# Kernel tuning notes

Hardware: AMD Instinct MI355X
Metric: run time of the kernel (lower is better)

## Reference

```python
import jax, jax.numpy as jnp
import numpy as np

N, C, H = 256, 128, 4
D = C // H


def setup_inputs() -> dict:
    key = jax.random.key(0)
    ks = jax.random.split(key, 7)
    pair_rep = jax.random.normal(ks[0], (N, N, C), dtype=jnp.float32)
    distance_matrix = jax.random.normal(ks[1], (N, N), dtype=jnp.float32)
    Wqkv = jax.random.normal(ks[2], (C, 3 * C), dtype=jnp.float32) * (1.0 / np.sqrt(C))
    bqkv = jax.random.normal(ks[3], (3 * C,), dtype=jnp.float32) * 0.02
    Wout = jax.random.normal(ks[4], (C, C), dtype=jnp.float32) * (1.0 / np.sqrt(C))
    bout = jax.random.normal(ks[5], (C,), dtype=jnp.float32) * 0.02
    dscale = jnp.ones((1,), dtype=jnp.float32)
    mask = jax.random.randint(ks[6], (N, N), 0, 2).astype(jnp.bool_)
    return {"pair_rep": pair_rep, "distance_matrix": distance_matrix, "Wqkv": Wqkv,
            "bqkv": bqkv, "Wout": Wout, "bout": bout, "dscale": dscale, "mask": mask}


def reference(pair_rep, distance_matrix, Wqkv, bqkv, Wout, bout, dscale, mask):
    n = pair_rep.shape[0]
    qkv = pair_rep @ Wqkv + bqkv                      # [n,n,3c]
    q, k, v = jnp.split(qkv, 3, axis=-1)
    q = q.reshape(n, n, H, D)
    k = k.reshape(n, n, H, D)
    v = v.reshape(n, n, H, D)
    # scores[h,i,j,k] = q[i,j,h,:] . k[i,k,h,:] / sqrt(D)
    scores = jnp.einsum('ijhd,ikhd->hijk', q, k) / np.sqrt(D)
    bias = (dscale[0] * distance_matrix)[None, None, :, :]   # [1,1,n,n]
    scores = scores + bias
    scores = jnp.where(mask[None, None, :, :], -jnp.inf, scores)
    attn = jax.nn.softmax(scores, axis=-1)            # [H,n,n,n]
    out = jnp.einsum('hijk,ikhd->ijhd', attn, v).reshape(n, n, C)
    return out @ Wout + bout
```

## Files before the change

kernel.cpp:

```cpp
#include <hip/hip_runtime.h>
#include <hip/hip_bf16.h>
#include <math.h>

#define NN 256
#define CC 128
#define HH 4
#define DD 32

typedef uint4 u128;
typedef __bf16 bf16x8 __attribute__((ext_vector_type(8)));
typedef float f32x4 __attribute__((ext_vector_type(4)));

#define LOG2E 1.4426950408889634f
#define QSC (0.17677669529663687f * LOG2E)

__global__ __launch_bounds__(256) void prep_kernel(
    const float* __restrict__ dm, const int* __restrict__ mask,
    const float* __restrict__ dscale,
    const float* __restrict__ Wqkv, const float* __restrict__ Wout,
    float* __restrict__ biasM,
    __hip_bfloat16* __restrict__ Wt_qkv, __hip_bfloat16* __restrict__ Wt_out)
{
    const int b = blockIdx.x, t = threadIdx.x;
    if (b < 256) {
        int idx = b * 256 + t;
        biasM[idx] = mask[idx] ? -INFINITY : dscale[0] * dm[idx] * LOG2E;
    } else if (b < 448) {
        int idx = (b - 256) * 256 + t;
        int n = idx >> 7, k = idx & 127;
        Wt_qkv[idx] = __float2bfloat16(Wqkv[(size_t)k * 384 + n]);
    } else {
        int idx = (b - 448) * 256 + t;
        int n = idx >> 7, k = idx & 127;
        Wt_out[idx] = __float2bfloat16(Wout[(size_t)k * CC + n]);
    }
}

__global__ __launch_bounds__(512, 4) void qkv_mfma_kernel(
    const float* __restrict__ A,
    const __hip_bfloat16* __restrict__ Bt,
    const float* __restrict__ bias,
    __hip_bfloat16* __restrict__ out)
{
    __shared__ __align__(16) __hip_bfloat16 As[128][136];
    __shared__ __align__(16) __hip_bfloat16 Bs[96][136];
    const int t = threadIdx.x;
    const int m0 = blockIdx.x * 128;
    const int n0 = blockIdx.y * 96;

    #pragma unroll
    for (int it = 0; it < 8; ++it) {
        int idx = it * 512 + t;
        int r = idx >> 5, c4 = (idx & 31) * 4;
        float4 v = *(const float4*)(A + (size_t)(m0 + r) * CC + c4);
        __hip_bfloat162 a01 = __float22bfloat162_rn(float2{v.x, v.y});
        __hip_bfloat162 a23 = __float22bfloat162_rn(float2{v.z, v.w});
        uint2 pk;
        pk.x = *(unsigned int*)&a01;
        pk.y = *(unsigned int*)&a23;
        *(uint2*)&As[r][c4] = pk;
    }
    #pragma unroll
    for (int it = 0; it < 3; ++it) {
        int idx = it * 512 + t;
        int n = idx >> 4, c8 = (idx & 15) * 8;
        *(u128*)&Bs[n][c8] = *(const u128*)(Bt + (size_t)(n0 + n) * CC + c8);
    }
    __syncthreads();

    const int w = t >> 6, lane = t & 63;
    const int n16 = lane & 15, quad = lane >> 4;
    const int mw = (w & 3) * 32, nw = (w >> 2) * 48;

    bf16x8 pf[2][4];
    #pragma unroll
    for (int mt = 0; mt < 2; ++mt)
        #pragma unroll
        for (int ks = 0; ks < 4; ++ks)
            pf[mt][ks] = *(const bf16x8*)&As[mw + mt * 16 + n16][ks * 32 + quad * 8];

    f32x4 acc[2][3];
    #pragma unroll
    for (int mt = 0; mt < 2; ++mt)
        #pragma unroll
        for (int nt = 0; nt < 3; ++nt) acc[mt][nt] = (f32x4){0.f, 0.f, 0.f, 0.f};

    #pragma unroll
    for (int nt = 0; nt < 3; ++nt) {
        bf16x8 wf[4];
        #pragma unroll
        for (int ks = 0; ks < 4; ++ks)
            wf[ks] = *(const bf16x8*)&Bs[nw + nt * 16 + n16][ks * 32 + quad * 8];
        #pragma unroll
        for (int ks = 0; ks < 4; ++ks)
            #pragma unroll
            for (int mt = 0; mt < 2; ++mt)
                acc[mt][nt] = __builtin_amdgcn_mfma_f32_16x16x32_bf16(wf[ks], pf[mt][ks], acc[mt][nt], 0, 0, 0);
    }

    #pragma unroll
    for (int nt = 0; nt < 3; ++nt) {
        int nbase = n0 + nw + nt * 16 + quad * 4;
        float4 b4 = *(const float4*)(bias + nbase);
        float sc = (nbase < CC) ? QSC : 1.0f;
        #pragma unroll
        for (int mt = 0; mt < 2; ++mt) {
            int m = m0 + mw + mt * 16 + n16;
            __hip_bfloat162 h01 = __float22bfloat162_rn(float2{(acc[mt][nt][0] + b4.x) * sc, (acc[mt][nt][1] + b4.y) * sc});
            __hip_bfloat162 h23 = __float22bfloat162_rn(float2{(acc[mt][nt][2] + b4.z) * sc, (acc[mt][nt][3] + b4.w) * sc});
            uint2 pk;
            pk.x = *(unsigned int*)&h01;
            pk.y = *(unsigned int*)&h23;
            *(uint2*)&out[(size_t)m * 384 + nbase] = pk;
        }
    }
}

__global__ __launch_bounds__(512, 4) void attn_mfma_kernel(
    const __hip_bfloat16* __restrict__ qkv,
    const float* __restrict__ biasM,
    __hip_bfloat16* __restrict__ attn_out)
{
    __shared__ __align__(16) __hip_bfloat16 Ks[NN][40];
    __shared__ __align__(16) __hip_bfloat16 VTs[DD][264];
    __shared__ __align__(16) __hip_bfloat16 Ps[8][16][136];

    const int bi = blockIdx.x;
    const int i = bi >> 2, h = bi & 3;
    const int t = threadIdx.x;

    if (t < NN) {
        const __hip_bfloat16* base = qkv + (size_t)(i * NN + t) * 384 + h * DD;
        const u128* ksrc = (const u128*)(base + CC);
        const u128* vsrc = (const u128*)(base + 2 * CC);
        u128* kdst = (u128*)&Ks[t][0];
        u128 vr[4];
        #pragma unroll
        for (int u = 0; u < 4; ++u) { kdst[u] = ksrc[u]; vr[u] = vsrc[u]; }
        const __hip_bfloat16* vh = (const __hip_bfloat16*)vr;
        #pragma unroll
        for (int d = 0; d < DD; ++d) VTs[d][t] = vh[d];
    }
    __syncthreads();

    const int w = t >> 6, lane = t & 63;
    const int n16 = lane & 15, quad = lane >> 4;

    for (int jt = 0; jt < 2; ++jt) {
        const int j0 = w * 32 + jt * 16;
        const int j = j0 + n16;

        bf16x8 qa = *(const bf16x8*)(qkv + (size_t)(i * NN + j) * 384 + h * DD + quad * 8);
        const float4* brow = (const float4*)(biasM + (size_t)j * NN);

        f32x4 s[16];
        #pragma unroll
        for (int kt = 0; kt < 16; ++kt) {
            bf16x8 kb = *(const bf16x8*)&Ks[kt * 16 + n16][quad * 8];
            float4 b4 = brow[kt * 4 + quad];
            s[kt] = __builtin_amdgcn_mfma_f32_16x16x32_bf16(
                kb, qa, (f32x4){b4.x, b4.y, b4.z, b4.w}, 0, 0, 0);
        }

        f32x4 sm = {0.f, 0.f, 0.f, 0.f};
        f32x4 o[2] = {(f32x4){0.f, 0.f, 0.f, 0.f}, (f32x4){0.f, 0.f, 0.f, 0.f}};
        #pragma unroll
        for (int pass = 0; pass < 2; ++pass) {
            #pragma unroll
            for (int kt8 = 0; kt8 < 8; ++kt8) {
                int kt = pass * 8 + kt8;
                float p0 = exp2f(s[kt][0]);
                float p1 = exp2f(s[kt][1]);
                float p2 = exp2f(s[kt][2]);
                float p3 = exp2f(s[kt][3]);
                sm[0] += p0; sm[1] += p1; sm[2] += p2; sm[3] += p3;
                __hip_bfloat162 h01 = __float22bfloat162_rn(float2{p0, p1});
                __hip_bfloat162 h23 = __float22bfloat162_rn(float2{p2, p3});
                uint2 pk;
                pk.x = *(unsigned int*)&h01;
                pk.y = *(unsigned int*)&h23;
                *(uint2*)&Ps[w][n16][kt8 * 16 + quad * 4] = pk;
            }
            #pragma unroll
            for (int c = 0; c < 4; ++c) {
                bf16x8 pa = *(const bf16x8*)&Ps[w][n16][c * 32 + quad * 8];
                #pragma unroll
                for (int dt = 0; dt < 2; ++dt) {
                    bf16x8 vb = *(const bf16x8*)&VTs[dt * 16 + n16][pass * 128 + c * 32 + quad * 8];
                    o[dt] = __builtin_amdgcn_mfma_f32_16x16x32_bf16(vb, pa, o[dt], 0, 0, 0);
                }
            }
        }
        float sum = (sm[0] + sm[1]) + (sm[2] + sm[3]);
        sum += __shfl_xor(sum, 16);
        sum += __shfl_xor(sum, 32);
        float inv = 1.0f / sum;

        __hip_bfloat16* obase = attn_out + (size_t)(i * NN + j) * CC + h * DD + quad * 4;
        #pragma unroll
        for (int dt = 0; dt < 2; ++dt) {
            __hip_bfloat162 h01 = __float22bfloat162_rn(float2{o[dt][0] * inv, o[dt][1] * inv});
            __hip_bfloat162 h23 = __float22bfloat162_rn(float2{o[dt][2] * inv, o[dt][3] * inv});
            uint2 pk;
            pk.x = *(unsigned int*)&h01;
            pk.y = *(unsigned int*)&h23;
            *(uint2*)(obase + dt * 16) = pk;
        }
    }
}

__global__ __launch_bounds__(512, 4) void out_mfma_kernel(
    const __hip_bfloat16* __restrict__ A,
    const __hip_bfloat16* __restrict__ Bt,
    const float* __restrict__ bias,
    float* __restrict__ out)
{
    __shared__ __align__(16) __hip_bfloat16 As[128][136];
    __shared__ __align__(16) __hip_bfloat16 Bs[128][136];
    const int t = threadIdx.x;
    const int m0 = blockIdx.x * 128;

    #pragma unroll
    for (int it = 0; it < 4; ++it) {
        int idx = it * 512 + t;
        int r = idx >> 4, c8 = (idx & 15) * 8;
        *(u128*)&As[r][c8] = *(const u128*)(A + (size_t)(m0 + r) * CC + c8);
    }
    #pragma unroll
    for (int it = 0; it < 4; ++it) {
        int idx = it * 512 + t;
        int n = idx >> 4, c8 = (idx & 15) * 8;
        *(u128*)&Bs[n][c8] = *(const u128*)(Bt + (size_t)n * CC + c8);
    }
    __syncthreads();

    const int w = t >> 6, lane = t & 63;
    const int n16 = lane & 15, quad = lane >> 4;
    const int mw = (w & 3) * 32, nw = (w >> 2) * 64;

    bf16x8 pf[2][4];
    #pragma unroll
    for (int mt = 0; mt < 2; ++mt)
        #pragma unroll
        for (int ks = 0; ks < 4; ++ks)
            pf[mt][ks] = *(const bf16x8*)&As[mw + mt * 16 + n16][ks * 32 + quad * 8];

    f32x4 acc[2][4];
    #pragma unroll
    for (int mt = 0; mt < 2; ++mt)
        #pragma unroll
        for (int nt = 0; nt < 4; ++nt) acc[mt][nt] = (f32x4){0.f, 0.f, 0.f, 0.f};

    #pragma unroll
    for (int nt = 0; nt < 4; ++nt) {
        bf16x8 wf[4];
        #pragma unroll
        for (int ks = 0; ks < 4; ++ks)
            wf[ks] = *(const bf16x8*)&Bs[nw + nt * 16 + n16][ks * 32 + quad * 8];
        #pragma unroll
        for (int ks = 0; ks < 4; ++ks)
            #pragma unroll
            for (int mt = 0; mt < 2; ++mt)
                acc[mt][nt] = __builtin_amdgcn_mfma_f32_16x16x32_bf16(wf[ks], pf[mt][ks], acc[mt][nt], 0, 0, 0);
    }

    #pragma unroll
    for (int nt = 0; nt < 4; ++nt) {
        int nbase = nw + nt * 16 + quad * 4;
        float4 b4 = *(const float4*)(bias + nbase);
        #pragma unroll
        for (int mt = 0; mt < 2; ++mt) {
            int m = m0 + mw + mt * 16 + n16;
            float4 ov;
            ov.x = acc[mt][nt][0] + b4.x;
            ov.y = acc[mt][nt][1] + b4.y;
            ov.z = acc[mt][nt][2] + b4.z;
            ov.w = acc[mt][nt][3] + b4.w;
            *(float4*)&out[(size_t)m * CC + nbase] = ov;
        }
    }
}

extern "C" void kernel_launch(void* const* d_in, const int* in_sizes, int n_in,
                              void* d_out, int out_size, void* d_ws, size_t ws_size,
                              hipStream_t stream) {
    const float* pair_rep = (const float*)d_in[0];
    const float* dm       = (const float*)d_in[1];
    const float* Wqkv     = (const float*)d_in[2];
    const float* bqkv     = (const float*)d_in[3];
    const float* Wout     = (const float*)d_in[4];
    const float* bout     = (const float*)d_in[5];
    const float* dscale   = (const float*)d_in[6];
    const int*   mask     = (const int*)d_in[7];
    float* out = (float*)d_out;

    char* p = (char*)d_ws;
    float* biasM = (float*)p;                 p += (size_t)NN * NN * 4;
    __hip_bfloat16* Wt_qkv = (__hip_bfloat16*)p;  p += (size_t)384 * CC * 2;
    __hip_bfloat16* Wt_out = (__hip_bfloat16*)p;  p += (size_t)CC * CC * 2;
    __hip_bfloat16* qkv  = (__hip_bfloat16*)p;    p += (size_t)65536 * 384 * 2;
    __hip_bfloat16* attn = (__hip_bfloat16*)p;

    prep_kernel<<<dim3(512), dim3(256), 0, stream>>>(dm, mask, dscale, Wqkv, Wout, biasM, Wt_qkv, Wt_out);
    qkv_mfma_kernel<<<dim3(512, 4), dim3(512), 0, stream>>>(pair_rep, Wt_qkv, bqkv, qkv);
    attn_mfma_kernel<<<dim3(1024), dim3(512), 0, stream>>>(qkv, biasM, attn);
    out_mfma_kernel<<<dim3(512), dim3(512), 0, stream>>>(attn, Wt_out, bout, out);
}
```

Measured before the change: 173.3 us.

## Shrink GEMM tiles, read weights from global directly, parallelize K/V staging

The QKV and output projection kernels now use 64-row tiles with 256 threads and twice as many blocks. Weight fragments are loaded straight from global memory (L2/L1-cached) instead of being staged in shared memory, which cuts LDS usage and removes a staging pass. The attention kernel now loads K/V with all 512 threads, two per row, instead of half the block, and unrolls the jt loop. The trade-off is more repeated global weight reads across blocks and less reuse of each weight fragment across row tiles.

```diff
diff --git a/kernel.cpp b/kernel.cpp
--- a/kernel.cpp
+++ b/kernel.cpp
@@ -36,21 +36,20 @@
     }
 }
 
-__global__ __launch_bounds__(512, 4) void qkv_mfma_kernel(
+__global__ __launch_bounds__(256) void qkv_mfma_kernel(
     const float* __restrict__ A,
     const __hip_bfloat16* __restrict__ Bt,
     const float* __restrict__ bias,
     __hip_bfloat16* __restrict__ out)
 {
-    __shared__ __align__(16) __hip_bfloat16 As[128][136];
-    __shared__ __align__(16) __hip_bfloat16 Bs[96][136];
+    __shared__ __align__(16) __hip_bfloat16 As[64][136];
     const int t = threadIdx.x;
-    const int m0 = blockIdx.x * 128;
+    const int m0 = blockIdx.x * 64;
     const int n0 = blockIdx.y * 96;
 
     #pragma unroll
     for (int it = 0; it < 8; ++it) {
-        int idx = it * 512 + t;
+        int idx = it * 256 + t;
         int r = idx >> 5, c4 = (idx & 31) * 4;
         float4 v = *(const float4*)(A + (size_t)(m0 + r) * CC + c4);
         __hip_bfloat162 a01 = __float22bfloat162_rn(float2{v.x, v.y});
@@ -60,59 +59,43 @@
         pk.y = *(unsigned int*)&a23;
         *(uint2*)&As[r][c4] = pk;
     }
-    #pragma unroll
-    for (int it = 0; it < 3; ++it) {
-        int idx = it * 512 + t;
-        int n = idx >> 4, c8 = (idx & 15) * 8;
-        *(u128*)&Bs[n][c8] = *(const u128*)(Bt + (size_t)(n0 + n) * CC + c8);
-    }
     __syncthreads();
 
     const int w = t >> 6, lane = t & 63;
     const int n16 = lane & 15, quad = lane >> 4;
-    const int mw = (w & 3) * 32, nw = (w >> 2) * 48;
-
-    bf16x8 pf[2][4];
-    #pragma unroll
-    for (int mt = 0; mt < 2; ++mt)
-        #pragma unroll
-        for (int ks = 0; ks < 4; ++ks)
-            pf[mt][ks] = *(const bf16x8*)&As[mw + mt * 16 + n16][ks * 32 + quad * 8];
-
-    f32x4 acc[2][3];
-    #pragma unroll
-    for (int mt = 0; mt < 2; ++mt)
-        #pragma unroll
-        for (int nt = 0; nt < 3; ++nt) acc[mt][nt] = (f32x4){0.f, 0.f, 0.f, 0.f};
-
-    #pragma unroll
-    for (int nt = 0; nt < 3; ++nt) {
-        bf16x8 wf[4];
-        #pragma unroll
-        for (int ks = 0; ks < 4; ++ks)
-            wf[ks] = *(const bf16x8*)&Bs[nw + nt * 16 + n16][ks * 32 + quad * 8];
-        #pragma unroll
-        for (int ks = 0; ks < 4; ++ks)
-            #pragma unroll
-            for (int mt = 0; mt < 2; ++mt)
-                acc[mt][nt] = __builtin_amdgcn_mfma_f32_16x16x32_bf16(wf[ks], pf[mt][ks], acc[mt][nt], 0, 0, 0);
-    }
-
-    #pragma unroll
-    for (int nt = 0; nt < 3; ++nt) {
-        int nbase = n0 + nw + nt * 16 + quad * 4;
+    const int mw = w * 16;
+
+    bf16x8 pf[4];
+    #pragma unroll
+    for (int ks = 0; ks < 4; ++ks)
+        pf[ks] = *(const bf16x8*)&As[mw + n16][ks * 32 + quad * 8];
+
+    f32x4 acc[6];
+    #pragma unroll
+    for (int nt = 0; nt < 6; ++nt) acc[nt] = (f32x4){0.f, 0.f, 0.f, 0.f};
+
+    #pragma unroll
+    for (int nt = 0; nt < 6; ++nt) {
+        const __hip_bfloat16* brow = Bt + (size_t)(n0 + nt * 16 + n16) * CC;
+        #pragma unroll
+        for (int ks = 0; ks < 4; ++ks) {
+            bf16x8 wf = *(const bf16x8*)(brow + ks * 32 + quad * 8);
+            acc[nt] = __builtin_amdgcn_mfma_f32_16x16x32_bf16(wf, pf[ks], acc[nt], 0, 0, 0);
+        }
+    }
+
+    #pragma unroll
+    for (int nt = 0; nt < 6; ++nt) {
+        int nbase = n0 + nt * 16 + quad * 4;
         float4 b4 = *(const float4*)(bias + nbase);
         float sc = (nbase < CC) ? QSC : 1.0f;
-        #pragma unroll
-        for (int mt = 0; mt < 2; ++mt) {
-            int m = m0 + mw + mt * 16 + n16;
-            __hip_bfloat162 h01 = __float22bfloat162_rn(float2{(acc[mt][nt][0] + b4.x) * sc, (acc[mt][nt][1] + b4.y) * sc});
-            __hip_bfloat162 h23 = __float22bfloat162_rn(float2{(acc[mt][nt][2] + b4.z) * sc, (acc[mt][nt][3] + b4.w) * sc});
-            uint2 pk;
-            pk.x = *(unsigned int*)&h01;
-            pk.y = *(unsigned int*)&h23;
-            *(uint2*)&out[(size_t)m * 384 + nbase] = pk;
-        }
+        int m = m0 + mw + n16;
+        __hip_bfloat162 h01 = __float22bfloat162_rn(float2{(acc[nt][0] + b4.x) * sc, (acc[nt][1] + b4.y) * sc});
+        __hip_bfloat162 h23 = __float22bfloat162_rn(float2{(acc[nt][2] + b4.z) * sc, (acc[nt][3] + b4.w) * sc});
+        uint2 pk;
+        pk.x = *(unsigned int*)&h01;
+        pk.y = *(unsigned int*)&h23;
+        *(uint2*)&out[(size_t)m * 384 + nbase] = pk;
     }
 }
 
@@ -129,23 +112,28 @@
     const int i = bi >> 2, h = bi & 3;
     const int t = threadIdx.x;
 
-    if (t < NN) {
-        const __hip_bfloat16* base = qkv + (size_t)(i * NN + t) * 384 + h * DD;
+    {
+        const int r = t >> 1, c = t & 1;
+        const __hip_bfloat16* base = qkv + (size_t)(i * NN + r) * 384 + h * DD;
         const u128* ksrc = (const u128*)(base + CC);
         const u128* vsrc = (const u128*)(base + 2 * CC);
-        u128* kdst = (u128*)&Ks[t][0];
-        u128 vr[4];
-        #pragma unroll
-        for (int u = 0; u < 4; ++u) { kdst[u] = ksrc[u]; vr[u] = vsrc[u]; }
-        const __hip_bfloat16* vh = (const __hip_bfloat16*)vr;
-        #pragma unroll
-        for (int d = 0; d < DD; ++d) VTs[d][t] = vh[d];
+        u128 k0 = ksrc[2 * c], k1 = ksrc[2 * c + 1];
+        u128 v0 = vsrc[2 * c], v1 = vsrc[2 * c + 1];
+        u128* kdst = (u128*)&Ks[r][0];
+        kdst[2 * c] = k0;
+        kdst[2 * c + 1] = k1;
+        __align__(16) __hip_bfloat16 vh[16];
+        *(u128*)&vh[0] = v0;
+        *(u128*)&vh[8] = v1;
+        #pragma unroll
+        for (int e = 0; e < 16; ++e) VTs[c * 16 + e][r] = vh[e];
     }
     __syncthreads();
 
     const int w = t >> 6, lane = t & 63;
     const int n16 = lane & 15, quad = lane >> 4;
 
+    #pragma unroll
     for (int jt = 0; jt < 2; ++jt) {
         const int j0 = w * 32 + jt * 16;
         const int j = j0 + n16;
@@ -209,75 +197,58 @@
     }
 }
 
-__global__ __launch_bounds__(512, 4) void out_mfma_kernel(
+__global__ __launch_bounds__(256) void out_mfma_kernel(
     const __hip_bfloat16* __restrict__ A,
     const __hip_bfloat16* __restrict__ Bt,
     const float* __restrict__ bias,
     float* __restrict__ out)
 {
-    __shared__ __align__(16) __hip_bfloat16 As[128][136];
-    __shared__ __align__(16) __hip_bfloat16 Bs[128][136];
+    __shared__ __align__(16) __hip_bfloat16 As[64][136];
     const int t = threadIdx.x;
-    const int m0 = blockIdx.x * 128;
+    const int m0 = blockIdx.x * 64;
 
     #pragma unroll
     for (int it = 0; it < 4; ++it) {
-        int idx = it * 512 + t;
+        int idx = it * 256 + t;
         int r = idx >> 4, c8 = (idx & 15) * 8;
         *(u128*)&As[r][c8] = *(const u128*)(A + (size_t)(m0 + r) * CC + c8);
     }
-    #pragma unroll
-    for (int it = 0; it < 4; ++it) {
-        int idx = it * 512 + t;
-        int n = idx >> 4, c8 = (idx & 15) * 8;
-        *(u128*)&Bs[n][c8] = *(const u128*)(Bt + (size_t)n * CC + c8);
-    }
     __syncthreads();
 
     const int w = t >> 6, lane = t & 63;
     const int n16 = lane & 15, quad = lane >> 4;
-    const int mw = (w & 3) * 32, nw = (w >> 2) * 64;
-
-    bf16x8 pf[2][4];
-    #pragma unroll
-    for (int mt = 0; mt < 2; ++mt)
-        #pragma unroll
-        for (int ks = 0; ks < 4; ++ks)
-            pf[mt][ks] = *(const bf16x8*)&As[mw + mt * 16 + n16][ks * 32 + quad * 8];
-
-    f32x4 acc[2][4];
-    #pragma unroll
-    for (int mt = 0; mt < 2; ++mt)
-        #pragma unroll
-        for (int nt = 0; nt < 4; ++nt) acc[mt][nt] = (f32x4){0.f, 0.f, 0.f, 0.f};
-
-    #pragma unroll
-    for (int nt = 0; nt < 4; ++nt) {
-        bf16x8 wf[4];
-        #pragma unroll
-        for (int ks = 0; ks < 4; ++ks)
-            wf[ks] = *(const bf16x8*)&Bs[nw + nt * 16 + n16][ks * 32 + quad * 8];
-        #pragma unroll
-        for (int ks = 0; ks < 4; ++ks)
-            #pragma unroll
-            for (int mt = 0; mt < 2; ++mt)
-                acc[mt][nt] = __builtin_amdgcn_mfma_f32_16x16x32_bf16(wf[ks], pf[mt][ks], acc[mt][nt], 0, 0, 0);
-    }
-
-    #pragma unroll
-    for (int nt = 0; nt < 4; ++nt) {
-        int nbase = nw + nt * 16 + quad * 4;
+    const int mw = w * 16;
+
+    bf16x8 pf[4];
+    #pragma unroll
+    for (int ks = 0; ks < 4; ++ks)
+        pf[ks] = *(const bf16x8*)&As[mw + n16][ks * 32 + quad * 8];
+
+    f32x4 acc[8];
+    #pragma unroll
+    for (int nt = 0; nt < 8; ++nt) acc[nt] = (f32x4){0.f, 0.f, 0.f, 0.f};
+
+    #pragma unroll
+    for (int nt = 0; nt < 8; ++nt) {
+        const __hip_bfloat16* brow = Bt + (size_t)(nt * 16 + n16) * CC;
+        #pragma unroll
+        for (int ks = 0; ks < 4; ++ks) {
+            bf16x8 wf = *(const bf16x8*)(brow + ks * 32 + quad * 8);
+            acc[nt] = __builtin_amdgcn_mfma_f32_16x16x32_bf16(wf, pf[ks], acc[nt], 0, 0, 0);
+        }
+    }
+
+    #pragma unroll
+    for (int nt = 0; nt < 8; ++nt) {
+        int nbase = nt * 16 + quad * 4;
         float4 b4 = *(const float4*)(bias + nbase);
-        #pragma unroll
-        for (int mt = 0; mt < 2; ++mt) {
-            int m = m0 + mw + mt * 16 + n16;
-            float4 ov;
-            ov.x = acc[mt][nt][0] + b4.x;
-            ov.y = acc[mt][nt][1] + b4.y;
-            ov.z = acc[mt][nt][2] + b4.z;
-            ov.w = acc[mt][nt][3] + b4.w;
-            *(float4*)&out[(size_t)m * CC + nbase] = ov;
-        }
+        int m = m0 + mw + n16;
+        float4 ov;
+        ov.x = acc[nt][0] + b4.x;
+        ov.y = acc[nt][1] + b4.y;
+        ov.z = acc[nt][2] + b4.z;
+        ov.w = acc[nt][3] + b4.w;
+        *(float4*)&out[(size_t)m * CC + nbase] = ov;
     }
 }
 
@@ -302,7 +273,7 @@
     __hip_bfloat16* attn = (__hip_bfloat16*)p;
 
     prep_kernel<<<dim3(512), dim3(256), 0, stream>>>(dm, mask, dscale, Wqkv, Wout, biasM, Wt_qkv, Wt_out);
-    qkv_mfma_kernel<<<dim3(512, 4), dim3(512), 0, stream>>>(pair_rep, Wt_qkv, bqkv, qkv);
+    qkv_mfma_kernel<<<dim3(1024, 4), dim3(256), 0, stream>>>(pair_rep, Wt_qkv, bqkv, qkv);
     attn_mfma_kernel<<<dim3(1024), dim3(512), 0, stream>>>(qkv, biasM, attn);
-    out_mfma_kernel<<<dim3(512), dim3(512), 0, stream>>>(attn, Wt_out, bout, out);
-}
+    out_mfma_kernel<<<dim3(1024), dim3(256), 0, stream>>>(attn, Wt_out, bout, out);
+}
```

After: 219.5 us. +26.7%, slower.
